# Kernel tuning notes

Hardware: AMD Instinct MI355X
Metric: run time of the kernel (lower is better)

Reference implementation:

```python
import jax, jax.numpy as jnp
import numpy as np

V, E, H, DV = 32000, 128, 512, 256
B, NV, MAXLEN = 128, 196, 32
TEMP, TOP_P = 0.8, 0.9


def setup_inputs() -> dict:
    key = jax.random.key(0)
    ks = jax.random.split(key, 22)
    def n(k, shape, s=0.02):
        return jax.random.normal(k, shape, dtype=jnp.float32) * s
    return {
        'thought': n(ks[0], (B, H), 1.0),
        'visual_features': n(ks[1], (B, NV, DV), 1.0),
        'emb': n(ks[2], (V, E)),
        'w_ih0': n(ks[3], (4 * H, E)), 'w_hh0': n(ks[4], (4 * H, H)),
        'b_ih0': n(ks[5], (4 * H,)), 'b_hh0': n(ks[6], (4 * H,)),
        'w_ih1': n(ks[7], (4 * H, H)), 'w_hh1': n(ks[8], (4 * H, H)),
        'b_ih1': n(ks[9], (4 * H,)), 'b_hh1': n(ks[10], (4 * H,)),
        'gw1': n(ks[11], (H, H)), 'gb1': n(ks[12], (H,)),
        'gw2': n(ks[13], (1, H)), 'gb2': n(ks[14], (1,)),
        'out_w': n(ks[15], (V, H)), 'out_b': n(ks[16], (V,)),
        'vis_w': n(ks[17], (H, DV)), 'vis_b': n(ks[18], (H,)),
        'ln_g': jnp.ones((H,), jnp.float32), 'ln_b': jnp.zeros((H,), jnp.float32),
        'max_len': MAXLEN,
    }


def _lstm_cell(x, h, c, wih, whh, bih, bhh):
    z = x @ wih.T + bih + h @ whh.T + bhh  # [B, 4H]
    i, f, g, o = jnp.split(z, 4, axis=-1)
    c2 = jax.nn.sigmoid(f) * c + jax.nn.sigmoid(i) * jnp.tanh(g)
    h2 = jax.nn.sigmoid(o) * jnp.tanh(c2)
    return h2, c2


def reference(thought, visual_features, emb, w_ih0, w_hh0, b_ih0, b_hh0,
              w_ih1, w_hh1, b_ih1, b_hh1, gw1, gb1, gw2, gb2,
              out_w, out_b, vis_w, vis_b, ln_g, ln_b, max_len):
    Bsz, Hd = thought.shape
    Vsz = out_w.shape[0]
    # visual projection + LayerNorm (dropout is identity at eval)
    vp = visual_features @ vis_w.T + vis_b  # [B, N, H]
    mu = vp.mean(-1, keepdims=True)
    var = vp.var(-1, keepdims=True)
    vp = (vp - mu) * jax.lax.rsqrt(var + 1e-5) * ln_g + ln_b

    key = jax.random.key(42)
    zeros = jnp.zeros_like(thought)
    tok0 = jnp.ones((Bsz,), jnp.int32)              # start token = 1
    hist0 = -jnp.ones((Bsz, 3), jnp.int32)          # last-3 token history (sentinel -1)
    carry0 = (thought, zeros, thought, zeros, tok0, hist0)
    rows = jnp.arange(Bsz)[:, None]

    def step(carry, step_idx):
        h0, c0, h1, c1, tok, hist = carry
        x = emb[tok]                                 # [B, E]
        h0, c0 = _lstm_cell(x, h0, c0, w_ih0, w_hh0, b_ih0, b_hh0)
        h1, c1 = _lstm_cell(h0, h1, c1, w_ih1, w_hh1, b_ih1, b_hh1)
        gate = jax.nn.sigmoid(jnp.tanh(h1 @ gw1.T + gb1) @ gw2.T + gb2)  # [B,1]
        o = h1 * gate
        # visual attention (single query per step)
        scores = jnp.einsum('bh,bnh->bn', o, vp) / (Hd ** 0.5)
        aw = jax.nn.softmax(scores, axis=-1)
        o = o + jnp.einsum('bn,bnh->bh', aw, vp)
        logits = o @ out_w.T + out_b                 # [B, V]
        # repetition penalty: -2.0 on each distinct token in last 3 (set semantics)
        m = jax.nn.one_hot(hist, Vsz, dtype=bool).any(axis=1)  # [B, V]
        logits = logits - 2.0 * m
        logits = logits / TEMP
        # top-p nucleus filtering
        order = jnp.argsort(-logits, axis=-1)
        sl = jnp.take_along_axis(logits, order, axis=-1)
        cum = jnp.cumsum(jax.nn.softmax(sl, axis=-1), axis=-1)
        rm = cum > TOP_P
        rm = jnp.concatenate([jnp.zeros_like(rm[:, :1]), rm[:, :-1]], axis=-1)
        rm_orig = jnp.zeros_like(rm).at[rows, order].set(rm)
        logits = jnp.where(rm_orig, -jnp.inf, logits)
        k = jax.random.fold_in(key, step_idx)
        nxt = jax.random.categorical(k, logits).astype(jnp.int32)
        hist = jnp.concatenate([hist[:, 1:], nxt[:, None]], axis=1)
        return (h0, c0, h1, c1, nxt, hist), nxt

    _, toks = jax.lax.scan(step, carry0, jnp.arange(int(max_len)))
    return toks.T  # [B, max_len]
```

## Files before the change

### kernel.cpp

```cpp
#include <hip/hip_runtime.h>
#include <stdint.h>

#define NB 128
#define NH 512
#define NE 128
#define NVOC 32000
#define NNV 196
#define NDV 256
#define NSTEPS 32
#define SORTSTRIDE 32768

static __device__ __forceinline__ uint32_t rotl32(uint32_t x, int r){
  return (x << r) | (x >> (32 - r));
}

static __device__ __forceinline__ void threefry2x32(uint32_t k0, uint32_t k1,
    uint32_t x0, uint32_t x1, uint32_t &o0, uint32_t &o1){
  uint32_t k2 = k0 ^ k1 ^ 0x1BD11BDAu;
  x0 += k0; x1 += k1;
#define TF_RND(r) { x0 += x1; x1 = rotl32(x1,(r)); x1 ^= x0; }
  TF_RND(13) TF_RND(15) TF_RND(26) TF_RND(6)
  x0 += k1; x1 += k2 + 1u;
  TF_RND(17) TF_RND(29) TF_RND(16) TF_RND(24)
  x0 += k2; x1 += k0 + 2u;
  TF_RND(13) TF_RND(15) TF_RND(26) TF_RND(6)
  x0 += k0; x1 += k1 + 3u;
  TF_RND(17) TF_RND(29) TF_RND(16) TF_RND(24)
  x0 += k1; x1 += k2 + 4u;
  TF_RND(13) TF_RND(15) TF_RND(26) TF_RND(6)
  x0 += k2; x1 += k0 + 5u;
#undef TF_RND
  o0 = x0; o1 = x1;
}

__global__ __launch_bounds__(256) void k_visproj(
    const float* __restrict__ vf, const float* __restrict__ vis_w,
    const float* __restrict__ vis_b, const float* __restrict__ ln_g,
    const float* __restrict__ ln_b, float* __restrict__ vp)
{
  int bn = blockIdx.x;
  int tid = threadIdx.x;
  __shared__ float xs[NDV];
  __shared__ float red[256];
  const float* x = vf + (size_t)bn * NDV;
  xs[tid] = x[tid];
  __syncthreads();
  float out0, out1;
  {
    const float4* h4 = (const float4*)xs;
    const float4* w0 = (const float4*)(vis_w + (size_t)tid * NDV);
    const float4* w1 = (const float4*)(vis_w + (size_t)(tid + 256) * NDV);
    float a0 = 0.f, a1 = 0.f;
    #pragma unroll 4
    for (int k = 0; k < NDV/4; k++){
      float4 hh = h4[k];
      float4 wa = w0[k], wb = w1[k];
      a0 = fmaf(hh.x, wa.x, a0); a0 = fmaf(hh.y, wa.y, a0);
      a0 = fmaf(hh.z, wa.z, a0); a0 = fmaf(hh.w, wa.w, a0);
      a1 = fmaf(hh.x, wb.x, a1); a1 = fmaf(hh.y, wb.y, a1);
      a1 = fmaf(hh.z, wb.z, a1); a1 = fmaf(hh.w, wb.w, a1);
    }
    out0 = a0 + vis_b[tid];
    out1 = a1 + vis_b[tid + 256];
  }
  red[tid] = out0 + out1; __syncthreads();
  for (int s = 128; s > 0; s >>= 1){ if (tid < s) red[tid] += red[tid + s]; __syncthreads(); }
  float mu = red[0] * (1.0f / (float)NH);
  __syncthreads();
  float d0 = out0 - mu, d1 = out1 - mu;
  red[tid] = d0*d0 + d1*d1; __syncthreads();
  for (int s = 128; s > 0; s >>= 1){ if (tid < s) red[tid] += red[tid + s]; __syncthreads(); }
  float var = red[0] * (1.0f / (float)NH);
  float r = 1.0f / sqrtf(var + 1e-5f);
  float* op = vp + (size_t)bn * NH;
  op[tid]       = d0 * r * ln_g[tid]       + ln_b[tid];
  op[tid + 256] = d1 * r * ln_g[tid + 256] + ln_b[tid + 256];
}

__global__ void k_init(const float* __restrict__ thought,
                       float* __restrict__ h0, float* __restrict__ c0,
                       float* __restrict__ h1, float* __restrict__ c1)
{
  int id = blockIdx.x * 256 + threadIdx.x;
  if (id >= NH * NB) return;
  int k = id >> 7;
  int b = id & 127;
  float v = thought[(size_t)b * NH + k];
  h0[id] = v; h1[id] = v; c0[id] = 0.f; c1[id] = 0.f;
}

template<int K1>
__global__ __launch_bounds__(256) void k_lstm(
    const float* __restrict__ wih, const float* __restrict__ whh,
    const float* __restrict__ bih, const float* __restrict__ bhh,
    const float* __restrict__ a1,
    const int*   __restrict__ toks, int step,
    const float* __restrict__ hprev, const float* __restrict__ cprev,
    float* __restrict__ hout, float* __restrict__ cout)
{
  __shared__ float As[64][64];
  __shared__ float Ws[4 * 16 * 68];
  __shared__ int tokl[64];
  int tid = threadIdx.x;
  int jl = tid & 15;
  int bg = tid >> 4;
  int jbase = blockIdx.x * 16;
  int j = jbase + jl;
  int bblk = blockIdx.y * 64;
  int bl = bg * 4;
  if (K1 == NE){
    if (tid < 64) tokl[tid] = (step == 0) ? 1 : toks[(size_t)(bblk + tid) * NSTEPS + step - 1];
  }
  __syncthreads();

  float acc[4][4];
  #pragma unroll
  for (int g = 0; g < 4; g++)
    #pragma unroll
    for (int e = 0; e < 4; e++) acc[g][e] = 0.f;

  for (int part = 0; part < 2; part++){
    const float* Wsrc = part ? whh : wih;
    const float* Asrc = part ? hprev : a1;
    const int K = part ? NH : K1;
    const bool gather = (!part) && (K1 == NE);
    for (int kc = 0; kc < K; kc += 64){
      __syncthreads();
      for (int q = tid; q < 1024; q += 256){
        int kk = q >> 4;
        int bb = (q & 15) << 2;
        float4 v;
        if (gather){
          v.x = Asrc[(size_t)tokl[bb+0] * NE + kc + kk];
          v.y = Asrc[(size_t)tokl[bb+1] * NE + kc + kk];
          v.z = Asrc[(size_t)tokl[bb+2] * NE + kc + kk];
          v.w = Asrc[(size_t)tokl[bb+3] * NE + kc + kk];
        } else {
          v = *(const float4*)(Asrc + (size_t)(kc + kk) * NB + bblk + bb);
        }
        *(float4*)&As[kk][bb] = v;
      }
      for (int q = tid; q < 1024; q += 256){
        int r = q >> 4;
        int f = q & 15;
        int g = r >> 4;
        int jj = r & 15;
        float4 w = *(const float4*)(Wsrc + (size_t)(g * NH + jbase + jj) * K + kc + f * 4);
        float* wd = &Ws[(g * 16 + jj) * 68 + f * 4];
        wd[0] = w.x; wd[1] = w.y; wd[2] = w.z; wd[3] = w.w;
      }
      __syncthreads();
      #pragma unroll 2
      for (int kk = 0; kk < 64; kk += 4){
        float4 a0 = *(const float4*)&As[kk + 0][bl];
        float4 a1v = *(const float4*)&As[kk + 1][bl];
        float4 a2 = *(const float4*)&As[kk + 2][bl];
        float4 a3 = *(const float4*)&As[kk + 3][bl];
        #pragma unroll
        for (int g = 0; g < 4; g++){
          float4 w = *(const float4*)&Ws[(g * 16 + jl) * 68 + kk];
          acc[g][0] = fmaf(a0.x, w.x, acc[g][0]);
          acc[g][1] = fmaf(a0.y, w.x, acc[g][1]);
          acc[g][2] = fmaf(a0.z, w.x, acc[g][2]);
          acc[g][3] = fmaf(a0.w, w.x, acc[g][3]);
          acc[g][0] = fmaf(a1v.x, w.y, acc[g][0]);
          acc[g][1] = fmaf(a1v.y, w.y, acc[g][1]);
          acc[g][2] = fmaf(a1v.z, w.y, acc[g][2]);
          acc[g][3] = fmaf(a1v.w, w.y, acc[g][3]);
          acc[g][0] = fmaf(a2.x, w.z, acc[g][0]);
          acc[g][1] = fmaf(a2.y, w.z, acc[g][1]);
          acc[g][2] = fmaf(a2.z, w.z, acc[g][2]);
          acc[g][3] = fmaf(a2.w, w.z, acc[g][3]);
          acc[g][0] = fmaf(a3.x, w.w, acc[g][0]);
          acc[g][1] = fmaf(a3.y, w.w, acc[g][1]);
          acc[g][2] = fmaf(a3.z, w.w, acc[g][2]);
          acc[g][3] = fmaf(a3.w, w.w, acc[g][3]);
        }
      }
    }
  }

  float bi[4];
  #pragma unroll
  for (int g = 0; g < 4; g++) bi[g] = bih[g * NH + j] + bhh[g * NH + j];
  int b0g = bblk + bl;
  float4 cp = *(const float4*)(cprev + (size_t)j * NB + b0g);
  float cpv[4] = {cp.x, cp.y, cp.z, cp.w};
  float hs[4], cs[4];
  #pragma unroll
  for (int e = 0; e < 4; e++){
    float zi = acc[0][e] + bi[0];
    float zf = acc[1][e] + bi[1];
    float zg = acc[2][e] + bi[2];
    float zo = acc[3][e] + bi[3];
    float si = 1.f / (1.f + expf(-zi));
    float sf = 1.f / (1.f + expf(-zf));
    float so = 1.f / (1.f + expf(-zo));
    float tg = tanhf(zg);
    float c2 = sf * cpv[e] + si * tg;
    cs[e] = c2;
    hs[e] = so * tanhf(c2);
  }
  *(float4*)(cout + (size_t)j * NB + b0g) = make_float4(cs[0], cs[1], cs[2], cs[3]);
  *(float4*)(hout + (size_t)j * NB + b0g) = make_float4(hs[0], hs[1], hs[2], hs[3]);
}

__global__ __launch_bounds__(256) void k_gateattn(
    const float* __restrict__ h1t,
    const float* __restrict__ gw1, const float* __restrict__ gb1,
    const float* __restrict__ gw2, const float* __restrict__ gb2,
    const float* __restrict__ vp,
    float* __restrict__ o2t)
{
  int b = blockIdx.x;
  int tid = threadIdx.x;
  __shared__ float hsm[NH];
  __shared__ float tsm[NH];
  __shared__ float osm[NH];
  __shared__ float aw[NNV];
  __shared__ float red[256];
  for (int h = tid; h < NH; h += 256) hsm[h] = h1t[(size_t)h * NB + b];
  __syncthreads();
  for (int jj = tid; jj < NH; jj += 256){
    const float4* wr = (const float4*)(gw1 + (size_t)jj * NH);
    const float4* h4 = (const float4*)hsm;
    float acc = 0.f;
    #pragma unroll 4
    for (int k = 0; k < NH/4; k++){
      float4 w = wr[k]; float4 hh = h4[k];
      acc = fmaf(hh.x, w.x, acc);
      acc = fmaf(hh.y, w.y, acc);
      acc = fmaf(hh.z, w.z, acc);
      acc = fmaf(hh.w, w.w, acc);
    }
    tsm[jj] = tanhf(acc + gb1[jj]);
  }
  __syncthreads();
  float part = 0.f;
  for (int jj = tid; jj < NH; jj += 256) part = fmaf(tsm[jj], gw2[jj], part);
  red[tid] = part; __syncthreads();
  for (int s = 128; s > 0; s >>= 1){ if (tid < s) red[tid] += red[tid + s]; __syncthreads(); }
  float gate = 1.f / (1.f + expf(-(red[0] + gb2[0])));
  __syncthreads();
  for (int h = tid; h < NH; h += 256) osm[h] = hsm[h] * gate;
  __syncthreads();
  const float* vpb = vp + (size_t)b * NNV * NH;
  float sc = 0.f;
  if (tid < NNV){
    const float4* vr = (const float4*)(vpb + (size_t)tid * NH);
    const float4* o4 = (const float4*)osm;
    float accv = 0.f;
    #pragma unroll 4
    for (int k = 0; k < NH/4; k++){
      float4 v = vr[k]; float4 oo = o4[k];
      accv = fmaf(oo.x, v.x, accv);
      accv = fmaf(oo.y, v.y, accv);
      accv = fmaf(oo.z, v.z, accv);
      accv = fmaf(oo.w, v.w, accv);
    }
    sc = accv / 22.62741699796952f;
  }
  red[tid] = (tid < NNV) ? sc : -INFINITY;
  __syncthreads();
  for (int s = 128; s > 0; s >>= 1){ if (tid < s) red[tid] = fmaxf(red[tid], red[tid + s]); __syncthreads(); }
  float mx = red[0];
  __syncthreads();
  float ev = (tid < NNV) ? expf(sc - mx) : 0.f;
  red[tid] = ev; __syncthreads();
  for (int s = 128; s > 0; s >>= 1){ if (tid < s) red[tid] += red[tid + s]; __syncthreads(); }
  float zs = red[0];
  if (tid < NNV) aw[tid] = ev / zs;
  __syncthreads();
  for (int h = tid; h < NH; h += 256){
    float accv = 0.f;
    for (int n = 0; n < NNV; n++) accv = fmaf(aw[n], vpb[(size_t)n * NH + h], accv);
    o2t[(size_t)h * NB + b] = osm[h] + accv;
  }
}

__global__ __launch_bounds__(256, 4) void k_logits(
    const float* __restrict__ o2t,
    const float* __restrict__ outw,
    const float* __restrict__ outb,
    const int* __restrict__ toks, int step,
    float* __restrict__ logits)
{
  __shared__ float osh[32][NB];
  __shared__ float wsh[32][72];
  __shared__ int hist[NB][3];
  int tid = threadIdx.x;
  int vbase = blockIdx.x * 64;
  int vl = (tid & 31) * 2;
  int b0 = (tid >> 5) * 16;
  if (tid < NB){
    hist[tid][0] = (step >= 1) ? toks[(size_t)tid * NSTEPS + step - 1] : -1;
    hist[tid][1] = (step >= 2) ? toks[(size_t)tid * NSTEPS + step - 2] : -1;
    hist[tid][2] = (step >= 3) ? toks[(size_t)tid * NSTEPS + step - 3] : -1;
  }
  float acc0[16], acc1[16];
  #pragma unroll
  for (int i = 0; i < 16; i++){ acc0[i] = 0.f; acc1[i] = 0.f; }

  for (int hc = 0; hc < NH; hc += 32){
    __syncthreads();
    #pragma unroll
    for (int q = tid; q < 1024; q += 256){
      int kk = q >> 5;
      int bb = (q & 31) << 2;
      *(float4*)&osh[kk][bb] = *(const float4*)(o2t + (size_t)(hc + kk) * NB + bb);
    }
    #pragma unroll
    for (int q = tid; q < 512; q += 256){
      int vr = q >> 3;
      int f4 = q & 7;
      float4 w = *(const float4*)(outw + (size_t)(vbase + vr) * NH + hc + f4 * 4);
      wsh[f4*4 + 0][vr] = w.x;
      wsh[f4*4 + 1][vr] = w.y;
      wsh[f4*4 + 2][vr] = w.z;
      wsh[f4*4 + 3][vr] = w.w;
    }
    __syncthreads();
    #pragma unroll 4
    for (int hl = 0; hl < 32; hl++){
      float w0 = wsh[hl][vl];
      float w1 = wsh[hl][vl + 1];
      #pragma unroll
      for (int bq = 0; bq < 4; bq++){
        float4 a = *(const float4*)&osh[hl][b0 + bq * 4];
        acc0[bq*4+0] = fmaf(a.x, w0, acc0[bq*4+0]);
        acc1[bq*4+0] = fmaf(a.x, w1, acc1[bq*4+0]);
        acc0[bq*4+1] = fmaf(a.y, w0, acc0[bq*4+1]);
        acc1[bq*4+1] = fmaf(a.y, w1, acc1[bq*4+1]);
        acc0[bq*4+2] = fmaf(a.z, w0, acc0[bq*4+2]);
        acc1[bq*4+2] = fmaf(a.z, w1, acc1[bq*4+2]);
        acc0[bq*4+3] = fmaf(a.w, w0, acc0[bq*4+3]);
        acc1[bq*4+3] = fmaf(a.w, w1, acc1[bq*4+3]);
      }
    }
  }
  __syncthreads();
  int v0 = vbase + vl;
  int v1 = v0 + 1;
  float ob0 = outb[v0], ob1 = outb[v1];
  #pragma unroll
  for (int i = 0; i < 16; i++){
    int b = b0 + i;
    float l0 = acc0[i] + ob0;
    float l1 = acc1[i] + ob1;
    int h1v = hist[b][0], h2v = hist[b][1], h3v = hist[b][2];
    if (v0 == h1v || v0 == h2v || v0 == h3v) l0 -= 2.0f;
    if (v1 == h1v || v1 == h2v || v1 == h3v) l1 -= 2.0f;
    l0 = l0 / 0.8f;
    l1 = l1 / 0.8f;
    *(float2*)(logits + (size_t)b * NVOC + v0) = make_float2(l0, l1);
  }
}

__global__ __launch_bounds__(1024) void k_sample(
    const float* __restrict__ logits,
    float* __restrict__ sortbuf,
    int* __restrict__ toks,
    int step)
{
  int b = blockIdx.x, tid = threadIdx.x;
  int lane = tid & 63, w = tid >> 6;
  const float* lrow = logits + (size_t)b * NVOC;
  float* B = sortbuf + (size_t)b * SORTSTRIDE;
  __shared__ __align__(16) float row[NVOC];
  __shared__ __align__(16) unsigned int offs[4096];
  __shared__ int wtot[16];
  __shared__ float sh_tval;
  __shared__ int sh_ckeep;

  float* ra = (float*)offs;
  if (tid < 256){
    const float4* lr4 = (const float4*)lrow;
    float mx = -INFINITY;
    for (int i = tid; i < NVOC/4; i += 256){
      float4 v = lr4[i];
      mx = fmaxf(mx, fmaxf(fmaxf(v.x, v.y), fmaxf(v.z, v.w)));
    }
    ra[tid] = mx;
  }
  __syncthreads();
  for (int s = 128; s > 0; s >>= 1){
    if (tid < s) ra[tid] = fmaxf(ra[tid], ra[tid + s]);
    __syncthreads();
  }
  float M = ra[0];
  __syncthreads();
  if (tid < 256){
    const float4* lr4 = (const float4*)lrow;
    float z = 0.f;
    for (int i = tid; i < NVOC/4; i += 256){
      float4 v = lr4[i];
      z += expf(v.x - M) + expf(v.y - M) + expf(v.z - M) + expf(v.w - M);
    }
    ra[tid] = z;
  }
  __syncthreads();
  for (int s = 128; s > 0; s >>= 1){
    if (tid < s) ra[tid] += ra[tid + s];
    __syncthreads();
  }
  float Z = ra[0];
  __syncthreads();

  int ebase = w * 2048;
  int qmax = (NVOC - ebase) >> 6;
  if (qmax > 32) qmax = 32;
  unsigned long long below = (1ull << lane) - 1ull;

  float vreg[32];
  unsigned int meta[32];

  for (int pass = 0; pass < 4; pass++){
    int sh = pass * 8;

    if (pass == 0){
      #pragma unroll
      for (int q = 0; q < 32; q++)
        if (q < qmax) vreg[q] = lrow[ebase + q * 64 + lane];
    } else {
      #pragma unroll
      for (int q = 0; q < 32; q++)
        if (q < qmax) vreg[q] = row[ebase + q * 64 + lane];
    }
    for (int i = tid; i < 4096; i += 1024) offs[i] = 0u;
    __syncthreads();

    #pragma unroll
    for (int q = 0; q < 32; q++){
      if (q < qmax){
        unsigned u = __float_as_uint(vreg[q]);
        unsigned key = ~(u ^ ((unsigned)(((int)u) >> 31) | 0x80000000u));
        unsigned d = (key >> sh) & 255u;
        unsigned long long m = ~0ull;
        #pragma unroll
        for (int bit = 0; bit < 8; bit++){
          unsigned long long bb = __ballot((d >> bit) & 1u);
          m &= ((d >> bit) & 1u) ? bb : ~bb;
        }
        int rank = __popcll(m & below);
        int cnt  = __popcll(m);
        meta[q] = d | ((unsigned)rank << 8) | ((unsigned)cnt << 14);
        if (rank == 0) offs[d * 16 + w] += (unsigned)cnt;
      }
    }
    __syncthreads();

    int fb = tid * 4;
    unsigned l0 = offs[fb], l1 = offs[fb+1], l2 = offs[fb+2], l3 = offs[fb+3];
    int v = (int)(l0 + l1 + l2 + l3);
    int inc = v;
    #pragma unroll
    for (int dd = 1; dd < 64; dd <<= 1){
      int o = __shfl_up(inc, dd);
      if (lane >= dd) inc += o;
    }
    if (lane == 63) wtot[w] = inc;
    __syncthreads();
    int woff = 0;
    #pragma unroll
    for (int ww = 0; ww < 16; ww++) woff += (ww < w) ? wtot[ww] : 0;
    unsigned run = (unsigned)(woff + inc - v);
    offs[fb]   = run; run += l0;
    offs[fb+1] = run; run += l1;
    offs[fb+2] = run; run += l2;
    offs[fb+3] = run;
    __syncthreads();

    #pragma unroll
    for (int q = 0; q < 32; q++){
      if (q < qmax){
        unsigned mt = meta[q];
        unsigned d = mt & 255u;
        int rank = (int)((mt >> 8) & 63u);
        unsigned cnt = mt >> 14;
        unsigned cur = offs[d * 16 + w];
        row[cur + rank] = vreg[q];
        if (rank == 0) offs[d * 16 + w] = cur + cnt;
      }
    }
    __syncthreads();
  }

  {
    float4* b4 = (float4*)B;
    for (int i = tid; i < NVOC / 4; i += 1024){
      float4 v = *(const float4*)&row[i * 4];
      b4[i] = v;
      float4 p;
      p.x = expf(v.x - M) / Z;
      p.y = expf(v.y - M) / Z;
      p.z = expf(v.z - M) / Z;
      p.w = expf(v.w - M) / Z;
      *(float4*)&row[i * 4] = p;
    }
  }
  __syncthreads();

  if (tid == 0){
    float s = 0.f, prev = 0.f;
    uint32_t base = (uint32_t)(uintptr_t)(void*)&row[0];
    uint32_t voff = base;
    uint32_t vend = base + (uint32_t)(NVOC * 4);

#define QBLK(R0,R1,R2,R3,RQ,OFF) \
  "s_waitcnt lgkmcnt(7)\n\t" \
  "v_add_f32 %[s], %[s], " R0 "\n\t" \
  "v_add_f32 %[s], %[s], " R1 "\n\t" \
  "v_add_f32 %[s], %[s], " R2 "\n\t" \
  "v_add_f32 %[s], %[s], " R3 "\n\t" \
  "ds_read_b128 " RQ ", %[voff] offset:" OFF "\n\t"

    asm volatile(
      "s_waitcnt lgkmcnt(0)\n\t"
      "ds_read_b128 v[40:43], %[voff] offset:0\n\t"
      "ds_read_b128 v[44:47], %[voff] offset:16\n\t"
      "ds_read_b128 v[48:51], %[voff] offset:32\n\t"
      "ds_read_b128 v[52:55], %[voff] offset:48\n\t"
      "ds_read_b128 v[56:59], %[voff] offset:64\n\t"
      "ds_read_b128 v[60:63], %[voff] offset:80\n\t"
      "ds_read_b128 v[64:67], %[voff] offset:96\n\t"
      "ds_read_b128 v[68:71], %[voff] offset:112\n\t"
      "Lscan%=:\n\t"
      "v_mov_b32 %[prev], %[s]\n\t"
      QBLK("v40","v41","v42","v43","v[40:43]","128")
      QBLK("v44","v45","v46","v47","v[44:47]","144")
      QBLK("v48","v49","v50","v51","v[48:51]","160")
      QBLK("v52","v53","v54","v55","v[52:55]","176")
      QBLK("v56","v57","v58","v59","v[56:59]","192")
      QBLK("v60","v61","v62","v63","v[60:63]","208")
      QBLK("v64","v65","v66","v67","v[64:67]","224")
      QBLK("v68","v69","v70","v71","v[68:71]","240")
      "v_add_u32 %[voff], 128, %[voff]\n\t"
      "v_cmp_lt_f32 vcc, 0x3f666666, %[s]\n\t"
      "s_cbranch_vccnz Ldone%=\n\t"
      "v_cmp_lt_u32 vcc, %[voff], %[vend]\n\t"
      "s_cbranch_vccnz Lscan%=\n\t"
      "Ldone%=:\n\t"
      "s_waitcnt lgkmcnt(0)\n\t"
      : [s]"+v"(s), [voff]"+v"(voff), [prev]"+v"(prev)
      : [vend]"v"(vend)
      : "vcc", "memory",
        "v40","v41","v42","v43","v44","v45","v46","v47",
        "v48","v49","v50","v51","v52","v53","v54","v55",
        "v56","v57","v58","v59","v60","v61","v62","v63",
        "v64","v65","v66","v67","v68","v69","v70","v71");
#undef QBLK

    int ks = NVOC - 1;
    if (s > 0.9f){
      int il0 = (int)((voff - base) >> 2) - 32;
      float t = prev;
      int kk = 31;
      for (int q = 0; q < 32; q++){
        t = t + row[il0 + q];
        if (t > 0.9f){ kk = q; break; }
      }
      ks = il0 + kk;
    }
    float tv = B[ks];
    int jlo = ks;
    while (jlo > 0 && B[jlo - 1] == tv) jlo--;
    sh_tval = tv;
    sh_ckeep = ks + 1 - jlo;
  }
  __syncthreads();

  float tval = sh_tval;
  int ckeep = sh_ckeep;
  float* redv = (float*)offs;
  int*   redi = (int*)(offs + 1024);

  int stt = tid * 32;
  int en = min(stt + 32, NVOC);
  int eqc = 0;
  for (int i = stt; i < en; i++) eqc += (lrow[i] == tval) ? 1 : 0;
  int inc = eqc;
  #pragma unroll
  for (int dd = 1; dd < 64; dd <<= 1){
    int o = __shfl_up(inc, dd);
    if (lane >= dd) inc += o;
  }
  if (lane == 63) wtot[w] = inc;
  __syncthreads();
  int woff = 0;
  #pragma unroll
  for (int ww = 0; ww < 16; ww++) woff += (ww < w) ? wtot[ww] : 0;
  int eqrank = woff + inc - eqc;

  uint32_t fk0, fk1;
  threefry2x32(0u, 42u, 0u, (uint32_t)step, fk0, fk1);
  float best = -INFINITY;
  int besti = NVOC;
  for (int i = stt; i < en; i++){
    float l = lrow[i];
    bool keep;
    if (l > tval) keep = true;
    else if (l == tval){ keep = (eqrank < ckeep); eqrank++; }
    else keep = false;
    if (keep){
      uint32_t o0, o1;
      threefry2x32(fk0, fk1, 0u, (uint32_t)(b * NVOC + i), o0, o1);
      uint32_t bits = o0 ^ o1;
      uint32_t fb2 = (bits >> 9) | 0x3f800000u;
      float u = __uint_as_float(fb2) - 1.0f;
      if (u == 0.0f) u = 1.17549435e-38f;
      float gum = -logf(-logf(u));
      float cand = l + gum;
      if (cand > best){ best = cand; besti = i; }
    }
  }
  redv[tid] = best;
  redi[tid] = besti;
  __syncthreads();
  for (int s = 512; s > 0; s >>= 1){
    if (tid < s){
      float ov = redv[tid + s]; int oi = redi[tid + s];
      if (ov > redv[tid] || (ov == redv[tid] && oi < redi[tid])){
        redv[tid] = ov; redi[tid] = oi;
      }
    }
    __syncthreads();
  }
  if (tid == 0) toks[(size_t)b * NSTEPS + step] = redi[0];
}

extern "C" void kernel_launch(void* const* d_in, const int* in_sizes, int n_in,
                              void* d_out, int out_size, void* d_ws, size_t ws_size,
                              hipStream_t stream)
{
  (void)in_sizes; (void)n_in; (void)out_size;
  const float* thought = (const float*)d_in[0];
  const float* vfeat   = (const float*)d_in[1];
  const float* emb     = (const float*)d_in[2];
  const float* w_ih0   = (const float*)d_in[3];
  const float* w_hh0   = (const float*)d_in[4];
  const float* b_ih0   = (const float*)d_in[5];
  const float* b_hh0   = (const float*)d_in[6];
  const float* w_ih1   = (const float*)d_in[7];
  const float* w_hh1   = (const float*)d_in[8];
  const float* b_ih1   = (const float*)d_in[9];
  const float* b_hh1   = (const float*)d_in[10];
  const float* gw1     = (const float*)d_in[11];
  const float* gb1     = (const float*)d_in[12];
  const float* gw2     = (const float*)d_in[13];
  const float* gb2     = (const float*)d_in[14];
  const float* out_w   = (const float*)d_in[15];
  const float* out_b   = (const float*)d_in[16];
  const float* vis_w   = (const float*)d_in[17];
  const float* vis_b   = (const float*)d_in[18];
  const float* ln_g    = (const float*)d_in[19];
  const float* ln_b    = (const float*)d_in[20];
  int* toks = (int*)d_out;

  char* ws = (char*)d_ws;
  size_t off = 0;
  auto alloc = [&](size_t bytes) -> void* {
    void* p = ws + off;
    off += (bytes + 255) & ~(size_t)255;
    return p;
  };
  float* vp      = (float*)alloc((size_t)NB * NNV * NH * 4);
  float* h0a     = (float*)alloc((size_t)NH * NB * 4);
  float* h0b     = (float*)alloc((size_t)NH * NB * 4);
  float* c0a     = (float*)alloc((size_t)NH * NB * 4);
  float* c0b     = (float*)alloc((size_t)NH * NB * 4);
  float* h1a     = (float*)alloc((size_t)NH * NB * 4);
  float* h1b     = (float*)alloc((size_t)NH * NB * 4);
  float* c1a     = (float*)alloc((size_t)NH * NB * 4);
  float* c1b     = (float*)alloc((size_t)NH * NB * 4);
  float* o2t     = (float*)alloc((size_t)NH * NB * 4);
  float* logits  = (float*)alloc((size_t)NB * NVOC * 4);
  float* sortbuf = (float*)alloc((size_t)NB * SORTSTRIDE * 4);
  if (off > ws_size) return;

  k_visproj<<<NB * NNV, 256, 0, stream>>>(vfeat, vis_w, vis_b, ln_g, ln_b, vp);
  k_init<<<(NH * NB + 255) / 256, 256, 0, stream>>>(thought, h0a, c0a, h1a, c1a);

  for (int step = 0; step < NSTEPS; step++){
    float *h0r, *h0w, *c0r, *c0w, *h1r, *h1w, *c1r, *c1w;
    if ((step & 1) == 0){
      h0r = h0a; h0w = h0b; c0r = c0a; c0w = c0b;
      h1r = h1a; h1w = h1b; c1r = c1a; c1w = c1b;
    } else {
      h0r = h0b; h0w = h0a; c0r = c0b; c0w = c0a;
      h1r = h1b; h1w = h1a; c1r = c1b; c1w = c1a;
    }
    k_lstm<NE><<<dim3(32, 2), 256, 0, stream>>>(
        w_ih0, w_hh0, b_ih0, b_hh0, emb, toks, step, h0r, c0r, h0w, c0w);
    k_lstm<NH><<<dim3(32, 2), 256, 0, stream>>>(
        w_ih1, w_hh1, b_ih1, b_hh1, h0w, toks, step, h1r, c1r, h1w, c1w);
    k_gateattn<<<NB, 256, 0, stream>>>(h1w, gw1, gb1, gw2, gb2, vp, o2t);
    k_logits<<<NVOC / 64, 256, 0, stream>>>(o2t, out_w, out_b, toks, step, logits);
    k_sample<<<NB, 1024, 0, stream>>>(logits, sortbuf, toks, step);
  }
}
```

Baseline: 21.41 ms.

## Replace per-row visual projection with tiled shared-memory GEMM plus separate LayerNorm

```diff
diff --git a/kernel.cpp b/kernel.cpp
--- a/kernel.cpp
+++ b/kernel.cpp
@@ -9,6 +9,7 @@
 #define NDV 256
 #define NSTEPS 32
 #define SORTSTRIDE 32768
+#define VTOK (NB * NNV)
 
 static __device__ __forceinline__ uint32_t rotl32(uint32_t x, int r){
   return (x << r) | (x >> (32 - r));
@@ -33,36 +34,83 @@
   o0 = x0; o1 = x1;
 }
 
-__global__ __launch_bounds__(256) void k_visproj(
-    const float* __restrict__ vf, const float* __restrict__ vis_w,
-    const float* __restrict__ vis_b, const float* __restrict__ ln_g,
-    const float* __restrict__ ln_b, float* __restrict__ vp)
+__global__ __launch_bounds__(256) void k_visgemm(
+    const float* __restrict__ vf,
+    const float* __restrict__ vis_w,
+    const float* __restrict__ vis_b,
+    float* __restrict__ vp)
+{
+  __shared__ float As[64][68];
+  __shared__ float Ws[64][68];
+  int tid = threadIdx.x;
+  int tx = tid & 15;
+  int ty = tid >> 4;
+  int mb = blockIdx.x * 64;
+  int hb = blockIdx.y * 64;
+  int m_l = ty * 4, h_l = tx * 4;
+
+  float acc[4][4];
+  #pragma unroll
+  for (int i = 0; i < 4; i++)
+    #pragma unroll
+    for (int j = 0; j < 4; j++) acc[i][j] = 0.f;
+
+  for (int kc = 0; kc < NDV; kc += 64){
+    __syncthreads();
+    for (int q = tid; q < 1024; q += 256){
+      int m = q >> 4, k4 = (q & 15) << 2;
+      *(float4*)&As[m][k4] = *(const float4*)(vf + (size_t)(mb + m) * NDV + kc + k4);
+    }
+    for (int q = tid; q < 1024; q += 256){
+      int h = q >> 4, k4 = (q & 15) << 2;
+      *(float4*)&Ws[h][k4] = *(const float4*)(vis_w + (size_t)(hb + h) * NDV + kc + k4);
+    }
+    __syncthreads();
+#define FMA4(i,j,av,wv) \
+    acc[i][j] = fmaf(av.x, wv.x, acc[i][j]); \
+    acc[i][j] = fmaf(av.y, wv.y, acc[i][j]); \
+    acc[i][j] = fmaf(av.z, wv.z, acc[i][j]); \
+    acc[i][j] = fmaf(av.w, wv.w, acc[i][j]);
+    #pragma unroll 4
+    for (int kk = 0; kk < 64; kk += 4){
+      float4 a0 = *(const float4*)&As[m_l + 0][kk];
+      float4 a1 = *(const float4*)&As[m_l + 1][kk];
+      float4 a2 = *(const float4*)&As[m_l + 2][kk];
+      float4 a3 = *(const float4*)&As[m_l + 3][kk];
+      float4 w0 = *(const float4*)&Ws[h_l + 0][kk];
+      float4 w1 = *(const float4*)&Ws[h_l + 1][kk];
+      float4 w2 = *(const float4*)&Ws[h_l + 2][kk];
+      float4 w3 = *(const float4*)&Ws[h_l + 3][kk];
+      FMA4(0,0,a0,w0) FMA4(0,1,a0,w1) FMA4(0,2,a0,w2) FMA4(0,3,a0,w3)
+      FMA4(1,0,a1,w0) FMA4(1,1,a1,w1) FMA4(1,2,a1,w2) FMA4(1,3,a1,w3)
+      FMA4(2,0,a2,w0) FMA4(2,1,a2,w1) FMA4(2,2,a2,w2) FMA4(2,3,a2,w3)
+      FMA4(3,0,a3,w0) FMA4(3,1,a3,w1) FMA4(3,2,a3,w2) FMA4(3,3,a3,w3)
+    }
+#undef FMA4
+  }
+
+  float4 bias = *(const float4*)(vis_b + hb + h_l);
+  #pragma unroll
+  for (int i = 0; i < 4; i++){
+    float4 o;
+    o.x = acc[i][0] + bias.x;
+    o.y = acc[i][1] + bias.y;
+    o.z = acc[i][2] + bias.z;
+    o.w = acc[i][3] + bias.w;
+    *(float4*)(vp + (size_t)(mb + m_l + i) * NH + hb + h_l) = o;
+  }
+}
+
+__global__ __launch_bounds__(256) void k_visln(
+    const float* __restrict__ ln_g, const float* __restrict__ ln_b,
+    float* __restrict__ vp)
 {
   int bn = blockIdx.x;
   int tid = threadIdx.x;
-  __shared__ float xs[NDV];
   __shared__ float red[256];
-  const float* x = vf + (size_t)bn * NDV;
-  xs[tid] = x[tid];
-  __syncthreads();
-  float out0, out1;
-  {
-    const float4* h4 = (const float4*)xs;
-    const float4* w0 = (const float4*)(vis_w + (size_t)tid * NDV);
-    const float4* w1 = (const float4*)(vis_w + (size_t)(tid + 256) * NDV);
-    float a0 = 0.f, a1 = 0.f;
-    #pragma unroll 4
-    for (int k = 0; k < NDV/4; k++){
-      float4 hh = h4[k];
-      float4 wa = w0[k], wb = w1[k];
-      a0 = fmaf(hh.x, wa.x, a0); a0 = fmaf(hh.y, wa.y, a0);
-      a0 = fmaf(hh.z, wa.z, a0); a0 = fmaf(hh.w, wa.w, a0);
-      a1 = fmaf(hh.x, wb.x, a1); a1 = fmaf(hh.y, wb.y, a1);
-      a1 = fmaf(hh.z, wb.z, a1); a1 = fmaf(hh.w, wb.w, a1);
-    }
-    out0 = a0 + vis_b[tid];
-    out1 = a1 + vis_b[tid + 256];
-  }
+  float* op = vp + (size_t)bn * NH;
+  float out0 = op[tid];
+  float out1 = op[tid + 256];
   red[tid] = out0 + out1; __syncthreads();
   for (int s = 128; s > 0; s >>= 1){ if (tid < s) red[tid] += red[tid + s]; __syncthreads(); }
   float mu = red[0] * (1.0f / (float)NH);
@@ -72,7 +120,6 @@
   for (int s = 128; s > 0; s >>= 1){ if (tid < s) red[tid] += red[tid + s]; __syncthreads(); }
   float var = red[0] * (1.0f / (float)NH);
   float r = 1.0f / sqrtf(var + 1e-5f);
-  float* op = vp + (size_t)bn * NH;
   op[tid]       = d0 * r * ln_g[tid]       + ln_b[tid];
   op[tid + 256] = d1 * r * ln_g[tid + 256] + ln_b[tid + 256];
 }
@@ -677,7 +724,8 @@
   float* sortbuf = (float*)alloc((size_t)NB * SORTSTRIDE * 4);
   if (off > ws_size) return;
 
-  k_visproj<<<NB * NNV, 256, 0, stream>>>(vfeat, vis_w, vis_b, ln_g, ln_b, vp);
+  k_visgemm<<<dim3(VTOK / 64, NH / 64), 256, 0, stream>>>(vfeat, vis_w, vis_b, vp);
+  k_visln<<<VTOK, 256, 0, stream>>>(ln_g, ln_b, vp);
   k_init<<<(NH * NB + 255) / 256, 256, 0, stream>>>(thought, h0a, c0a, h1a, c1a);
 
   for (int step = 0; step < NSTEPS; step++){
```

Measured after the change: 20.25 ms. 5.4% less time.
